# Kernel optimization log

Hardware: AMD Instinct MI355X
Metric: run time of the kernel (lower is better)

The kernel has to match this reference:

```python
import jax, jax.numpy as jnp
import numpy as np

B, T, D = 2, 2048, 4096
H, G, d = 32, 8, 128
GROUP = H // G  # 4


def setup_inputs() -> dict:
    key = jax.random.key(0)
    ks = jax.random.split(key, 9)
    s = 0.02
    return {
        "hidden_states": jax.random.normal(ks[0], (B, T, D), jnp.float32),
        "Wq": jax.random.normal(ks[1], (D, D), jnp.float32) * s,
        "bq": jax.random.normal(ks[2], (D,), jnp.float32) * s,
        "Wk": jax.random.normal(ks[3], (G * d, D), jnp.float32) * s,
        "bk": jax.random.normal(ks[4], (G * d,), jnp.float32) * s,
        "Wv": jax.random.normal(ks[5], (G * d, D), jnp.float32) * s,
        "bv": jax.random.normal(ks[6], (G * d,), jnp.float32) * s,
        "Wo": jax.random.normal(ks[7], (D, D), jnp.float32) * s,
        "bo": jax.random.normal(ks[8], (D,), jnp.float32) * s,
    }


def reference(hidden_states, Wq, bq, Wk, bk, Wv, bv, Wo, bo):
    # projections (torch Linear: x @ W.T + b)
    q = hidden_states @ Wq.T + bq            # [B,T,D]
    k = hidden_states @ Wk.T + bk            # [B,T,G*d]
    v = hidden_states @ Wv.T + bv            # [B,T,G*d]

    # [B,G,group,T,d] for q; [B,G,T,d] for k,v. repeat_interleave(group, dim=1)
    # on [B,H,...] is exactly the (G, group) grouping of heads.
    q = q.reshape(B, T, G, GROUP, d).transpose(0, 2, 3, 1, 4)  # bgptd
    k = k.reshape(B, T, G, d).transpose(0, 2, 1, 3)            # bgsd
    v = v.reshape(B, T, G, d).transpose(0, 2, 1, 3)            # bgsd

    scale = 1.0 / np.sqrt(d).astype(np.float32)
    scores = jnp.einsum("bgptd,bgsd->bgpts", q, k) * scale     # [B,G,group,Tq,Tk]

    # causal additive mask: (j > i) * -1e9  (past_len = 0)
    i = jnp.arange(T)[:, None]
    j = jnp.arange(T)[None, :]
    causal_add = (j > i).astype(scores.dtype) * -1e9
    scores = scores + causal_add               # broadcast over b,g,p

    attn = jax.nn.softmax(scores, axis=-1)
    y = jnp.einsum("bgpts,bgsd->bgptd", attn, v)               # [B,G,group,T,d]
    y = y.transpose(0, 3, 1, 2, 4).reshape(B, T, D)            # [B,T,H*d]
    return y @ Wo.T + bo
```

## Files before the change

kernel.cpp:

```cpp
#include <hip/hip_runtime.h>
#include <hip/hip_bf16.h>
#include <cstdint>
#include <cstddef>

using bf16 = __hip_bfloat16;
typedef __attribute__((ext_vector_type(8))) short bf16x8;
typedef __attribute__((ext_vector_type(4))) float floatx4;

#define GLOBAL_AS __attribute__((address_space(1)))
#define LDS_AS    __attribute__((address_space(3)))

__device__ __forceinline__ void async_copy16(void* lds, const void* g) {
    __builtin_amdgcn_global_load_lds((GLOBAL_AS void*)(g), (LDS_AS void*)(lds), 16, 0, 0);
}

__device__ __forceinline__ floatx4 mfma_bf16(bf16x8 a, bf16x8 b, floatx4 c) {
    return __builtin_amdgcn_mfma_f32_16x16x32_bf16(a, b, c, 0, 0, 0);
}

__global__ void cvt_f32_bf16(const float* __restrict__ src, bf16* __restrict__ dst, int n) {
    int i = (blockIdx.x * blockDim.x + threadIdx.x) * 4;
    if (i < n) {
        float4 v = *(const float4*)(src + i);
        __align__(8) bf16 t[4];
        t[0] = __float2bfloat16(v.x);
        t[1] = __float2bfloat16(v.y);
        t[2] = __float2bfloat16(v.z);
        t[3] = __float2bfloat16(v.w);
        *(short4*)(dst + i) = *(const short4*)t;
    }
}

template <int OUTF>
__global__ __launch_bounds__(256, 3) void gemm_bt_bias(
    const bf16* __restrict__ A, const bf16* __restrict__ W,
    const float* __restrict__ bias, void* __restrict__ Cv,
    int M, int N, int K)
{
    __shared__ __align__(16) bf16 As[128 * 32];
    __shared__ __align__(16) bf16 Ws[128 * 32];

    const int tid  = threadIdx.x;
    const int lane = tid & 63;
    const int wave = tid >> 6;
    const int quad = lane >> 4;
    const int l16  = lane & 15;
    const int wm = (wave >> 1) * 64;
    const int wn = (wave & 1) * 64;

    const int bm = blockIdx.x;
    const int bn = blockIdx.y;

    floatx4 acc[4][4];
#pragma unroll
    for (int i = 0; i < 4; ++i)
#pragma unroll
        for (int j = 0; j < 4; ++j) acc[i][j] = (floatx4){0.f, 0.f, 0.f, 0.f};

    const int srow = tid >> 2;
    const int scol = (tid & 3) * 8;
    const bf16* gA = A + (size_t)(bm * 128 + srow) * K + scol;
    const bf16* gW = W + (size_t)(bn * 128 + srow) * K + scol;
    bf16* lA0 = As + tid * 8;
    bf16* lA1 = As + 2048 + tid * 8;
    bf16* lW0 = Ws + tid * 8;
    bf16* lW1 = Ws + 2048 + tid * 8;
    const size_t skip = (size_t)64 * K;

    const int kt_n = K >> 5;
    for (int kt = 0; kt < kt_n; ++kt) {
        __syncthreads();
        const bf16* ga = gA + kt * 32;
        const bf16* gw = gW + kt * 32;
        async_copy16(lA0, ga);
        async_copy16(lA1, ga + skip);
        async_copy16(lW0, gw);
        async_copy16(lW1, gw + skip);
        __syncthreads();

        bf16x8 af[4], bfr[4];
#pragma unroll
        for (int mi = 0; mi < 4; ++mi)
            af[mi] = *(const bf16x8*)(As + (wm + mi * 16 + l16) * 32 + quad * 8);
#pragma unroll
        for (int ni = 0; ni < 4; ++ni)
            bfr[ni] = *(const bf16x8*)(Ws + (wn + ni * 16 + l16) * 32 + quad * 8);
#pragma unroll
        for (int mi = 0; mi < 4; ++mi)
#pragma unroll
            for (int ni = 0; ni < 4; ++ni)
                acc[mi][ni] = mfma_bf16(af[mi], bfr[ni], acc[mi][ni]);
    }

#pragma unroll
    for (int mi = 0; mi < 4; ++mi) {
        const int row0 = bm * 128 + wm + mi * 16 + quad * 4;
#pragma unroll
        for (int ni = 0; ni < 4; ++ni) {
            const int col = bn * 128 + wn + ni * 16 + l16;
            const float bv = bias[col];
            if (OUTF) {
                float* C = (float*)Cv;
#pragma unroll
                for (int r = 0; r < 4; ++r)
                    C[(size_t)(row0 + r) * N + col] = acc[mi][ni][r] + bv;
            } else {
                bf16* C = (bf16*)Cv;
#pragma unroll
                for (int r = 0; r < 4; ++r)
                    C[(size_t)(row0 + r) * N + col] = __float2bfloat16(acc[mi][ni][r] + bv);
            }
        }
    }
}

__global__ __launch_bounds__(256, 3) void gemm_kv(
    const bf16* __restrict__ A,
    const bf16* __restrict__ Wk, const bf16* __restrict__ Wv,
    const float* __restrict__ bk, const float* __restrict__ bv,
    bf16* __restrict__ kout, bf16* __restrict__ vt,
    int M, int K)
{
    __shared__ __align__(16) bf16 As[128 * 32];
    __shared__ __align__(16) bf16 Ws[128 * 32];

    const int tid  = threadIdx.x;
    const int lane = tid & 63;
    const int wave = tid >> 6;
    const int quad = lane >> 4;
    const int l16  = lane & 15;
    const int wm = (wave >> 1) * 64;
    const int wn = (wave & 1) * 64;

    const int bm = blockIdx.x;
    const int bn = blockIdx.y;
    const bool isK = (bn < 8);
    const int nb = isK ? bn : (bn - 8);
    const bf16* Wsel  = isK ? Wk : Wv;
    const float* bsel = isK ? bk : bv;

    floatx4 acc[4][4];
#pragma unroll
    for (int i = 0; i < 4; ++i)
#pragma unroll
        for (int j = 0; j < 4; ++j) acc[i][j] = (floatx4){0.f, 0.f, 0.f, 0.f};

    const int srow = tid >> 2;
    const int scol = (tid & 3) * 8;
    const bf16* gA = A    + (size_t)(bm * 128 + srow) * K + scol;
    const bf16* gW = Wsel + (size_t)(nb * 128 + srow) * K + scol;
    bf16* lA0 = As + tid * 8;
    bf16* lA1 = As + 2048 + tid * 8;
    bf16* lW0 = Ws + tid * 8;
    bf16* lW1 = Ws + 2048 + tid * 8;
    const size_t skip = (size_t)64 * K;

    const int kt_n = K >> 5;
    for (int kt = 0; kt < kt_n; ++kt) {
        __syncthreads();
        const bf16* ga = gA + kt * 32;
        const bf16* gw = gW + kt * 32;
        async_copy16(lA0, ga);
        async_copy16(lA1, ga + skip);
        async_copy16(lW0, gw);
        async_copy16(lW1, gw + skip);
        __syncthreads();

        bf16x8 af[4], bfr[4];
#pragma unroll
        for (int mi = 0; mi < 4; ++mi)
            af[mi] = *(const bf16x8*)(As + (wm + mi * 16 + l16) * 32 + quad * 8);
#pragma unroll
        for (int ni = 0; ni < 4; ++ni)
            bfr[ni] = *(const bf16x8*)(Ws + (wn + ni * 16 + l16) * 32 + quad * 8);
#pragma unroll
        for (int mi = 0; mi < 4; ++mi)
#pragma unroll
            for (int ni = 0; ni < 4; ++ni)
                acc[mi][ni] = mfma_bf16(af[mi], bfr[ni], acc[mi][ni]);
    }

#pragma unroll
    for (int mi = 0; mi < 4; ++mi) {
        const int row0 = bm * 128 + wm + mi * 16 + quad * 4;
#pragma unroll
        for (int ni = 0; ni < 4; ++ni) {
            const int col = nb * 128 + wn + ni * 16 + l16;
            const float bvv = bsel[col];
            if (isK) {
#pragma unroll
                for (int r = 0; r < 4; ++r)
                    kout[(size_t)(row0 + r) * 1024 + col] = __float2bfloat16(acc[mi][ni][r] + bvv);
            } else {
                __align__(8) bf16 tmp[4];
#pragma unroll
                for (int r = 0; r < 4; ++r) tmp[r] = __float2bfloat16(acc[mi][ni][r] + bvv);
                const int b  = row0 >> 11;
                const int t0 = row0 & 2047;
                bf16* dst = vt + ((size_t)(b * 1024 + col)) * 2048 + t0;
                *(short4*)dst = *(const short4*)tmp;
            }
        }
    }
}

__global__ __launch_bounds__(256, 2) void attn_fwd(
    const bf16* __restrict__ qb, const bf16* __restrict__ kb,
    const bf16* __restrict__ vtb, bf16* __restrict__ ob)
{
    constexpr int T  = 2048;
    constexpr int DQ = 4096;
    constexpr int DK = 1024;

    __shared__ __align__(16) bf16 Qs[128][136];
    __shared__ __align__(16) bf16 Ks[64][136];
    __shared__ __align__(16) bf16 Vt[128][72];
    __shared__ __align__(16) bf16 Ps[4][16][72];

    const int tid  = threadIdx.x;
    const int lane = tid & 63;
    const int wave = tid >> 6;
    const int quad = lane >> 4;
    const int l16  = lane & 15;

    const int qi = blockIdx.x;
    const int bh = blockIdx.y;
    const int b  = bh >> 5;
    const int h  = bh & 31;
    const int g  = h >> 2;
    const int qtB = 31 - qi;
    const int qtA = qi;
    const int q0B = qtB * 64;
    const int q0A = qtA * 64;
    const int qw = wave * 16;

    const bf16* Qg = qb  + (size_t)b * T * DQ + (size_t)h * 128;
    const bf16* Kg = kb  + (size_t)b * T * DK + (size_t)g * 128;
    const bf16* Vg = vtb + ((size_t)b * DK + g * 128) * T;
    bf16*       Og = ob  + (size_t)b * T * DQ + (size_t)h * 128;

#pragma unroll
    for (int it = 0; it < 8; ++it) {
        int idx = it * 256 + tid;
        int r = idx >> 4, c = (idx & 15) * 8;
        int grow = (r < 64) ? (q0B + r) : (q0A + r - 64);
        *(int4*)&Qs[r][c] = *(const int4*)(Qg + (size_t)grow * DQ + c);
    }

    floatx4 oacc[2][8];
#pragma unroll
    for (int t = 0; t < 2; ++t)
#pragma unroll
        for (int i = 0; i < 8; ++i) oacc[t][i] = (floatx4){0.f, 0.f, 0.f, 0.f};
    float m_run[2][4], l_run[2][4];
#pragma unroll
    for (int t = 0; t < 2; ++t)
#pragma unroll
        for (int r = 0; r < 4; ++r) { m_run[t][r] = -1e30f; l_run[t][r] = 0.f; }

    const float scale = 0.08838834764831845f;

    for (int st = 0; st <= qtB; ++st) {
        const int s0 = st * 64;
        __syncthreads();
#pragma unroll
        for (int it = 0; it < 4; ++it) {
            int idx = it * 256 + tid;
            int r = idx >> 4, c = (idx & 15) * 8;
            *(int4*)&Ks[r][c] = *(const int4*)(Kg + (size_t)(s0 + r) * DK + c);
        }
#pragma unroll
        for (int it = 0; it < 4; ++it) {
            int idx = it * 256 + tid;
            int r = idx >> 3, c = (idx & 7) * 8;
            *(int4*)&Vt[r][c] = *(const int4*)(Vg + (size_t)r * T + s0 + c);
        }
        __syncthreads();

        const int ntile = (st <= qtA) ? 2 : 1;
#pragma unroll
        for (int t = 0; t < 2; ++t) {
            if (t >= ntile) break;
            const int q0t  = t ? q0A : q0B;
            const int qt_t = t ? qtA : qtB;
            const int rowbase = t * 64;

            floatx4 sacc[4];
#pragma unroll
            for (int i = 0; i < 4; ++i) sacc[i] = (floatx4){0.f, 0.f, 0.f, 0.f};
#pragma unroll
            for (int kk = 0; kk < 4; ++kk) {
                bf16x8 aq = *(const bf16x8*)&Qs[rowbase + qw + l16][kk * 32 + quad * 8];
#pragma unroll
                for (int ni = 0; ni < 4; ++ni) {
                    bf16x8 bk8 = *(const bf16x8*)&Ks[ni * 16 + l16][kk * 32 + quad * 8];
                    sacc[ni] = mfma_bf16(aq, bk8, sacc[ni]);
                }
            }

            const bool diag = (st == qt_t);
#pragma unroll
            for (int r = 0; r < 4; ++r) {
                const int qg = q0t + qw + quad * 4 + r;
                float sv[4];
#pragma unroll
                for (int ni = 0; ni < 4; ++ni) {
                    float x = sacc[ni][r] * scale;
                    if (diag && (s0 + ni * 16 + l16) > qg) x = -1e30f;
                    sv[ni] = x;
                }
                float mx = fmaxf(fmaxf(sv[0], sv[1]), fmaxf(sv[2], sv[3]));
                mx = fmaxf(mx, __shfl_xor(mx, 1, 64));
                mx = fmaxf(mx, __shfl_xor(mx, 2, 64));
                mx = fmaxf(mx, __shfl_xor(mx, 4, 64));
                mx = fmaxf(mx, __shfl_xor(mx, 8, 64));
                const float mnew  = fmaxf(m_run[t][r], mx);
                const float alpha = __expf(m_run[t][r] - mnew);
                float ssum = 0.f;
#pragma unroll
                for (int ni = 0; ni < 4; ++ni) {
                    float p = __expf(sv[ni] - mnew);
                    ssum += p;
                    Ps[wave][quad * 4 + r][ni * 16 + l16] = __float2bfloat16(p);
                }
                ssum += __shfl_xor(ssum, 1, 64);
                ssum += __shfl_xor(ssum, 2, 64);
                ssum += __shfl_xor(ssum, 4, 64);
                ssum += __shfl_xor(ssum, 8, 64);
                l_run[t][r] = l_run[t][r] * alpha + ssum;
                m_run[t][r] = mnew;
#pragma unroll
                for (int db = 0; db < 8; ++db) oacc[t][db][r] *= alpha;
            }
            asm volatile("s_waitcnt lgkmcnt(0)" ::: "memory");

#pragma unroll
            for (int kk = 0; kk < 2; ++kk) {
                bf16x8 ap = *(const bf16x8*)&Ps[wave][l16][kk * 32 + quad * 8];
#pragma unroll
                for (int db = 0; db < 8; ++db) {
                    bf16x8 bv8 = *(const bf16x8*)&Vt[db * 16 + l16][kk * 32 + quad * 8];
                    oacc[t][db] = mfma_bf16(ap, bv8, oacc[t][db]);
                }
            }
        }
    }

#pragma unroll
    for (int t = 0; t < 2; ++t) {
        const int q0t = t ? q0A : q0B;
#pragma unroll
        for (int r = 0; r < 4; ++r) {
            const float inv = 1.0f / l_run[t][r];
            const int qg = q0t + qw + quad * 4 + r;
#pragma unroll
            for (int db = 0; db < 8; ++db)
                Og[(size_t)qg * DQ + db * 16 + l16] = __float2bfloat16(oacc[t][db][r] * inv);
        }
    }
}

extern "C" void kernel_launch(void* const* d_in, const int* in_sizes, int n_in,
                              void* d_out, int out_size, void* d_ws, size_t ws_size,
                              hipStream_t stream)
{
    const float* hs = (const float*)d_in[0];
    const float* Wq = (const float*)d_in[1];
    const float* bq = (const float*)d_in[2];
    const float* Wk = (const float*)d_in[3];
    const float* bk = (const float*)d_in[4];
    const float* Wv = (const float*)d_in[5];
    const float* bv = (const float*)d_in[6];
    const float* Wo = (const float*)d_in[7];
    const float* bo = (const float*)d_in[8];
    float* out = (float*)d_out;

    const int M  = 4096;
    const int D  = 4096;
    const int DK = 1024;
    const size_t SZ_D  = (size_t)M * D;
    const size_t SZ_K  = (size_t)M * DK;

    bf16* hsb  = (bf16*)d_ws;
    bf16* Wqb  = hsb  + SZ_D;
    bf16* Wkb  = Wqb  + SZ_D;
    bf16* Wvb  = Wkb  + SZ_K;
    bf16* Wob  = Wvb  + SZ_K;
    bf16* q_buf = Wob + SZ_D;
    bf16* k_buf = q_buf + SZ_D;
    bf16* vt_buf = Wqb;
    bf16* o_buf  = hsb;

    dim3 blk(256);
    const int CB = 256;
    cvt_f32_bf16<<<(int)(SZ_D / 4 + CB - 1) / CB, CB, 0, stream>>>(hs, hsb, (int)SZ_D);
    cvt_f32_bf16<<<(int)(SZ_D / 4 + CB - 1) / CB, CB, 0, stream>>>(Wq, Wqb, (int)SZ_D);
    cvt_f32_bf16<<<(int)(SZ_K / 4 + CB - 1) / CB, CB, 0, stream>>>(Wk, Wkb, (int)SZ_K);
    cvt_f32_bf16<<<(int)(SZ_K / 4 + CB - 1) / CB, CB, 0, stream>>>(Wv, Wvb, (int)SZ_K);
    cvt_f32_bf16<<<(int)(SZ_D / 4 + CB - 1) / CB, CB, 0, stream>>>(Wo, Wob, (int)SZ_D);

    gemm_bt_bias<0><<<dim3(M / 128, D / 128), blk, 0, stream>>>(hsb, Wqb, bq, q_buf, M, D, D);
    gemm_kv<<<dim3(M / 128, 16), blk, 0, stream>>>(hsb, Wkb, Wvb, bk, bv, k_buf, vt_buf, M, D);
    attn_fwd<<<dim3(16, 64), blk, 0, stream>>>(q_buf, k_buf, vt_buf, o_buf);
    gemm_bt_bias<1><<<dim3(M / 128, D / 128), blk, 0, stream>>>(o_buf, Wob, bo, out, M, D, D);
}
```

Measured before the change: 820.9 us.

## Double-buffer K/V tiles with async LDS loads, keep Q in registers, swizzle LDS

The attention kernel now prefetches the next K/V tile into a second LDS buffer with global_load_lds async copies while the current tile is computed, and drops the synchronous per-tile loads. Q fragments are loaded once into registers instead of being staged through shared memory. Padded LDS rows are replaced by an XOR swizzle to avoid bank conflicts. The aim is to hide global-memory latency and cut LDS traffic. The cost is higher register pressure from the Q fragments and a single barrier per iteration, which depends on the async copy being complete at that barrier.

```diff
diff --git a/kernel.cpp b/kernel.cpp
--- a/kernel.cpp
+++ b/kernel.cpp
@@ -212,9 +212,8 @@
     constexpr int DQ = 4096;
     constexpr int DK = 1024;
 
-    __shared__ __align__(16) bf16 Qs[128][136];
-    __shared__ __align__(16) bf16 Ks[64][136];
-    __shared__ __align__(16) bf16 Vt[128][72];
+    __shared__ __align__(16) bf16 Ks[2][64 * 128];
+    __shared__ __align__(16) bf16 Vs[2][128 * 64];
     __shared__ __align__(16) bf16 Ps[4][16][72];
 
     const int tid  = threadIdx.x;
@@ -222,6 +221,7 @@
     const int wave = tid >> 6;
     const int quad = lane >> 4;
     const int l16  = lane & 15;
+    const int swz  = l16 & 7;
 
     const int qi = blockIdx.x;
     const int bh = blockIdx.y;
@@ -239,13 +239,39 @@
     const bf16* Vg = vtb + ((size_t)b * DK + g * 128) * T;
     bf16*       Og = ob  + (size_t)b * T * DQ + (size_t)h * 128;
 
-#pragma unroll
-    for (int it = 0; it < 8; ++it) {
-        int idx = it * 256 + tid;
-        int r = idx >> 4, c = (idx & 15) * 8;
-        int grow = (r < 64) ? (q0B + r) : (q0A + r - 64);
-        *(int4*)&Qs[r][c] = *(const int4*)(Qg + (size_t)grow * DQ + c);
-    }
+    bf16x8 qf[2][4];
+    {
+        const size_t rB = (size_t)(q0B + qw + l16) * DQ;
+        const size_t rA = (size_t)(q0A + qw + l16) * DQ;
+#pragma unroll
+        for (int kk = 0; kk < 4; ++kk) {
+            qf[0][kk] = *(const bf16x8*)(Qg + rB + kk * 32 + quad * 8);
+            qf[1][kk] = *(const bf16x8*)(Qg + rA + kk * 32 + quad * 8);
+        }
+    }
+
+    const int krow_l = tid >> 4;
+    const int kc16   = tid & 15;
+    const int vrow_l = tid >> 3;
+    const int vc16   = tid & 7;
+
+    auto STAGE = [&](int st_, int bi_) {
+        const int s0_ = st_ * 64;
+        bf16* kbp = &Ks[bi_][0];
+        bf16* vbp = &Vs[bi_][0];
+#pragma unroll
+        for (int i = 0; i < 4; ++i) {
+            const int r = i * 16 + krow_l;
+            async_copy16(kbp + (i * 256 + tid) * 8,
+                         Kg + (size_t)(s0_ + r) * DK + ((kc16 ^ (r & 7)) * 8));
+        }
+#pragma unroll
+        for (int i = 0; i < 4; ++i) {
+            const int r = i * 32 + vrow_l;
+            async_copy16(vbp + (i * 256 + tid) * 8,
+                         Vg + (size_t)r * T + s0_ + ((vc16 ^ (r & 7)) * 8));
+        }
+    };
 
     floatx4 oacc[2][8];
 #pragma unroll
@@ -260,22 +286,17 @@
 
     const float scale = 0.08838834764831845f;
 
+    STAGE(0, 0);
+    __syncthreads();
+
     for (int st = 0; st <= qtB; ++st) {
+        const int bi = st & 1;
         const int s0 = st * 64;
-        __syncthreads();
-#pragma unroll
-        for (int it = 0; it < 4; ++it) {
-            int idx = it * 256 + tid;
-            int r = idx >> 4, c = (idx & 15) * 8;
-            *(int4*)&Ks[r][c] = *(const int4*)(Kg + (size_t)(s0 + r) * DK + c);
-        }
-#pragma unroll
-        for (int it = 0; it < 4; ++it) {
-            int idx = it * 256 + tid;
-            int r = idx >> 3, c = (idx & 7) * 8;
-            *(int4*)&Vt[r][c] = *(const int4*)(Vg + (size_t)r * T + s0 + c);
-        }
-        __syncthreads();
+
+        if (st < qtB) STAGE(st + 1, bi ^ 1);
+
+        const bf16* Kb = &Ks[bi][0];
+        const bf16* Vb = &Vs[bi][0];
 
         const int ntile = (st <= qtA) ? 2 : 1;
 #pragma unroll
@@ -283,18 +304,17 @@
             if (t >= ntile) break;
             const int q0t  = t ? q0A : q0B;
             const int qt_t = t ? qtA : qtB;
-            const int rowbase = t * 64;
 
             floatx4 sacc[4];
 #pragma unroll
             for (int i = 0; i < 4; ++i) sacc[i] = (floatx4){0.f, 0.f, 0.f, 0.f};
 #pragma unroll
             for (int kk = 0; kk < 4; ++kk) {
-                bf16x8 aq = *(const bf16x8*)&Qs[rowbase + qw + l16][kk * 32 + quad * 8];
+                const int koff = ((kk * 4 + quad) ^ swz) * 8;
 #pragma unroll
                 for (int ni = 0; ni < 4; ++ni) {
-                    bf16x8 bk8 = *(const bf16x8*)&Ks[ni * 16 + l16][kk * 32 + quad * 8];
-                    sacc[ni] = mfma_bf16(aq, bk8, sacc[ni]);
+                    bf16x8 bk8 = *(const bf16x8*)(Kb + (ni * 16 + l16) * 128 + koff);
+                    sacc[ni] = mfma_bf16(qf[t][kk], bk8, sacc[ni]);
                 }
             }
 
@@ -337,13 +357,16 @@
 #pragma unroll
             for (int kk = 0; kk < 2; ++kk) {
                 bf16x8 ap = *(const bf16x8*)&Ps[wave][l16][kk * 32 + quad * 8];
+                const int voff = ((kk * 4 + quad) ^ swz) * 8;
 #pragma unroll
                 for (int db = 0; db < 8; ++db) {
-                    bf16x8 bv8 = *(const bf16x8*)&Vt[db * 16 + l16][kk * 32 + quad * 8];
+                    bf16x8 bv8 = *(const bf16x8*)(Vb + (db * 16 + l16) * 64 + voff);
                     oacc[t][db] = mfma_bf16(ap, bv8, oacc[t][db]);
                 }
             }
         }
+
+        __syncthreads();
     }
 
 #pragma unroll
```

Result: faster. 791.1 us (-3.6%).
